# Kernel optimization log

Measured on AMD Instinct MI355X. Metric: run time of the kernel, lower is better.

## Reference

```python
import jax, jax.numpy as jnp
import numpy as np

NX, NY = 8, 1
IN_DELAY, FB_DELAY = 3, 3
MAX_DELAY = max(IN_DELAY, FB_DELAY)
HID = 64
NT, NG = 4096, 1024
IN_FEAT = (NX - NY) * (IN_DELAY + 1) + NY * (FB_DELAY + 1)  # 32


def setup_inputs() -> dict:
    key = jax.random.key(0)
    ks = jax.random.split(key, 10)
    s = lambda *sh: 0.05
    return {
        "x": jax.random.normal(ks[0], (NT, NG, NX), jnp.float32),
        "W_in": jax.random.normal(ks[1], (HID, IN_FEAT), jnp.float32) * 0.1,
        "b_in": jax.random.normal(ks[2], (HID,), jnp.float32) * 0.1,
        "W_ih": jax.random.normal(ks[3], (HID, HID), jnp.float32) * 0.1,
        "b_ih": jax.random.normal(ks[4], (HID,), jnp.float32) * 0.1,
        "W_hh": jax.random.normal(ks[5], (HID, HID), jnp.float32) * 0.1,
        "b_hh": jax.random.normal(ks[6], (HID,), jnp.float32) * 0.1,
        "W_out": jax.random.normal(ks[7], (NY, HID), jnp.float32) * 0.1,
        "b_out": jax.random.normal(ks[8], (NY,), jnp.float32) * 0.1,
    }


def _narx_forward(x, W_in, b_in, W_ih, b_ih, b_hh, W_out, b_out):
    nt = x.shape[0]
    # Source concat order: x0_t = x0[-1] then all x0[i], i=0..delay-1 (last slice duplicated).
    # x0 spans times [t-delay, t-1], so offsets relative to t are:
    off_x = jnp.array([-1] + list(range(-IN_DELAY, 0)))   # [4]
    off_y = jnp.array([-1] + list(range(-FB_DELAY, 0)))   # [4]
    ts = jnp.arange(MAX_DELAY, nt)                          # [T']
    # Gather delay windows: [T', n_off, ngrid, feat] -> [T', ngrid, n_off*feat]
    xw = x[ts[:, None] + off_x[None, :], :, :NX - NY]
    xw = jnp.transpose(xw, (0, 2, 1, 3)).reshape(xw.shape[0], xw.shape[2], -1)
    yw = x[ts[:, None] + off_y[None, :], :, NX - NY:]
    yw = jnp.transpose(yw, (0, 2, 1, 3)).reshape(yw.shape[0], yw.shape[2], -1)
    xt = jnp.concatenate([xw, yw], axis=-1)                 # [T', ngrid, IN_FEAT]
    h = jax.nn.relu(jnp.einsum('tgi,hi->tgh', xt, W_in) + b_in)
    # RNNCell called with hx=None each step in the source -> hidden is zeros every
    # call (W_hh contributes nothing); out = tanh(W_ih h + b_ih + b_hh).
    a = jnp.tanh(jnp.einsum('tgh,oh->tgo', h, W_ih) + b_ih + b_hh)
    y = jnp.einsum('tgh,oh->tgo', a, W_out) + b_out         # [T', ngrid, NY]
    # out[:max_delay] = x[:max_delay, :, -ny:]
    return jnp.concatenate([x[:MAX_DELAY, :, NX - NY:], y], axis=0)


def reference(x, W_in, b_in, W_ih, b_ih, W_hh, b_hh, W_out, b_out):
    # NestedNarx applies the shared Narx dl_model to every basin's series; with
    # the batched Narx this is exactly one call over all basins.
    return _narx_forward(x, W_in, b_in, W_ih, b_ih, b_hh, W_out, b_out)
```

## Files before the change

### kernel.cpp

```cpp
#include <hip/hip_runtime.h>
#include <hip/hip_bf16.h>


typedef __attribute__((ext_vector_type(8))) short bf16x8;
typedef __attribute__((ext_vector_type(4))) float f32x4;

__device__ __forceinline__ unsigned pk2(float lo, float hi) {
    unsigned r;
    asm("v_cvt_pk_bf16_f32 %0, %1, %2" : "=v"(r) : "v"(lo), "v"(hi));
    return r;
}

union BF8 { bf16x8 v; unsigned u[4]; uint4 q; };


__global__ __launch_bounds__(64) void narx_prep(
    const float* __restrict__ W_in, const float* __restrict__ b_in,
    const float* __restrict__ W_ih, const float* __restrict__ b_ih,
    const float* __restrict__ b_hh, const float* __restrict__ W_out,
    uint4* __restrict__ ws)
{
    const int lane = threadIdx.x;
    const int c = lane >> 4, pl = lane & 15;

    #pragma unroll
    for (int T = 0; T < 4; ++T) {
        const int r = ((pl >> 2) * 8) + (pl & 3) + (T & 1) * 4 + (T >> 1) * 32;
        const float* W = W_in + r * 32;
        float wr[8];
        if (c == 0) {
            #pragma unroll
            for (int j = 0; j < 7; ++j) wr[j] = W[j] + W[21 + j];
            wr[7] = W[28] + W[31];
        } else if (c == 1) {
            #pragma unroll
            for (int j = 0; j < 7; ++j) wr[j] = W[14 + j];
            wr[7] = W[30];
        } else if (c == 2) {
            #pragma unroll
            for (int j = 0; j < 7; ++j) wr[j] = W[7 + j];
            wr[7] = W[29];
        } else {
            wr[0] = b_in[r];
            #pragma unroll
            for (int j = 1; j < 8; ++j) wr[j] = 0.0f;
        }
        BF8 t;
        t.u[0] = pk2(wr[0], wr[1]); t.u[1] = pk2(wr[2], wr[3]);
        t.u[2] = pk2(wr[4], wr[5]); t.u[3] = pk2(wr[6], wr[7]);
        ws[lane*4 + T] = t.q;
    }

    #pragma unroll
    for (int k0 = 0; k0 < 2; ++k0)
    #pragma unroll
    for (int U = 0; U < 4; ++U) {
        const int r = ((pl >> 2) * 8) + (pl & 3) + (U & 1) * 4 + (U >> 1) * 32;
        const float* p = W_ih + r * 64 + 32*k0 + 8*c;
        float4 u0 = *(const float4*)p, u1 = *(const float4*)(p + 4);
        BF8 t;
        t.u[0] = pk2(u0.x, u0.y); t.u[1] = pk2(u0.z, u0.w);
        t.u[2] = pk2(u1.x, u1.y); t.u[3] = pk2(u1.z, u1.w);
        ws[256 + lane*8 + k0*4 + U] = t.q;
    }

    float4* wsf = (float4*)ws;
    #pragma unroll
    for (int U = 0; U < 4; ++U) {
        const int o = 8*c + 4*(U & 1) + 32*(U >> 1);
        wsf[768 + lane*4 + U] = make_float4(b_ih[o+0]+b_hh[o+0], b_ih[o+1]+b_hh[o+1],
                                            b_ih[o+2]+b_hh[o+2], b_ih[o+3]+b_hh[o+3]);
    }

    #pragma unroll
    for (int k0 = 0; k0 < 2; ++k0) {
        BF8 t;
        if (pl == 0) {
            const float* p = W_out + 32*k0 + 8*c;
            t.u[0] = pk2(p[0], p[1]); t.u[1] = pk2(p[2], p[3]);
            t.u[2] = pk2(p[4], p[5]); t.u[3] = pk2(p[6], p[7]);
        } else {
            t.u[0] = t.u[1] = t.u[2] = t.u[3] = 0u;
        }
        ws[1280 + lane*2 + k0] = t.q;
    }
}

__global__ __launch_bounds__(256, 2) void narx_main(
    const float* __restrict__ x, const uint4* __restrict__ ws,
    const float* __restrict__ b_out, float* __restrict__ out)
{
    __shared__ unsigned short F[4][128][32];

    const int nwg  = gridDim.x;
    const int orig = blockIdx.x;
    const int q8 = nwg >> 3, r8 = nwg & 7;
    const int xcd = orig & 7, inner = orig >> 3;
    const int b = (xcd < r8 ? xcd * (q8 + 1) : r8 * (q8 + 1) + (xcd - r8) * q8) + inner;

    const int lane = threadIdx.x & 63;
    const int w    = threadIdx.x >> 6;
    const int c    = lane >> 4;
    const int pl   = lane & 15;
    const int pt0  = 3072 + b * 512 + w * 128;

    bf16x8 wa[4];
    #pragma unroll
    for (int T = 0; T < 4; ++T) { BF8 t; t.q = ws[lane*4 + T]; wa[T] = t.v; }
    bf16x8 wi[2][4];
    #pragma unroll
    for (int k0 = 0; k0 < 2; ++k0)
    #pragma unroll
    for (int U = 0; U < 4; ++U) { BF8 t; t.q = ws[256 + lane*8 + k0*4 + U]; wi[k0][U] = t.v; }
    bf16x8 woa[2];
    #pragma unroll
    for (int k0 = 0; k0 < 2; ++k0) { BF8 t; t.q = ws[1280 + lane*2 + k0]; woa[k0] = t.v; }
    const float4* wsf = (const float4*)ws;
    f32x4 bias2[4];
    #pragma unroll
    for (int U = 0; U < 4; ++U) {
        float4 v = wsf[768 + lane*4 + U];
        bias2[U] = f32x4{v.x, v.y, v.z, v.w};
    }
    const float bout = b_out[0];
    const f32x4 cy = {c == 0 ? bout : 0.f, 0.f, 0.f, 0.f};
    const f32x4 zero = {0.f, 0.f, 0.f, 0.f};

    const float4* xr = (const float4*)x;
    {
        const int p0 = pt0 + lane, p1 = pt0 + 64 + lane;
        const int t0 = p0 >> 10, g0v = p0 & 1023;
        const int t1 = p1 >> 10, g1v = p1 & 1023;
        const size_t a1 = ((size_t)(t0-1)*1024 + g0v)*2, a2 = ((size_t)(t0-2)*1024 + g0v)*2,
                     a3 = ((size_t)(t0-3)*1024 + g0v)*2;
        const size_t d1a = ((size_t)(t1-1)*1024 + g1v)*2, d2a = ((size_t)(t1-2)*1024 + g1v)*2,
                     d3a = ((size_t)(t1-3)*1024 + g1v)*2;
        float4 A0 = xr[a1],  A1 = xr[a1+1],  B0 = xr[a2],  B1 = xr[a2+1],
               C0 = xr[a3],  C1 = xr[a3+1];
        float4 D0 = xr[d1a], D1 = xr[d1a+1], E0 = xr[d2a], E1 = xr[d2a+1],
               G0 = xr[d3a], G1 = xr[d3a+1];
        const int s = (lane >> 1) & 3;
        uint4* Fr0 = (uint4*)&F[w][lane][0];
        Fr0[0 ^ s] = make_uint4(pk2(A0.x,A0.y), pk2(A0.z,A0.w), pk2(A1.x,A1.y), pk2(A1.z,A1.w));
        Fr0[1 ^ s] = make_uint4(pk2(B0.x,B0.y), pk2(B0.z,B0.w), pk2(B1.x,B1.y), pk2(B1.z,B1.w));
        Fr0[2 ^ s] = make_uint4(pk2(C0.x,C0.y), pk2(C0.z,C0.w), pk2(C1.x,C1.y), pk2(C1.z,C1.w));
        Fr0[3 ^ s] = make_uint4(0x00003f80u, 0u, 0u, 0u);
        uint4* Fr1 = (uint4*)&F[w][64 + lane][0];
        Fr1[0 ^ s] = make_uint4(pk2(D0.x,D0.y), pk2(D0.z,D0.w), pk2(D1.x,D1.y), pk2(D1.z,D1.w));
        Fr1[1 ^ s] = make_uint4(pk2(E0.x,E0.y), pk2(E0.z,E0.w), pk2(E1.x,E1.y), pk2(E1.z,E1.w));
        Fr1[2 ^ s] = make_uint4(pk2(G0.x,G0.y), pk2(G0.z,G0.w), pk2(G1.x,G1.y), pk2(G1.z,G1.w));
        Fr1[3 ^ s] = make_uint4(0x00003f80u, 0u, 0u, 0u);
    }
    asm volatile("s_waitcnt lgkmcnt(0)" ::: "memory");
    __builtin_amdgcn_sched_barrier(0);

    asm volatile("" : "+v"(wa[0]), "+v"(wa[1]), "+v"(wa[2]), "+v"(wa[3]),
                      "+v"(wi[0][0]), "+v"(wi[0][1]), "+v"(wi[0][2]), "+v"(wi[0][3]),
                      "+v"(wi[1][0]), "+v"(wi[1][1]), "+v"(wi[1][2]), "+v"(wi[1][3]),
                      "+v"(bias2[0]), "+v"(bias2[1]), "+v"(bias2[2]), "+v"(bias2[3]),
                      "+v"(woa[0]), "+v"(woa[1]));

    const int s_rd = (pl >> 1) & 3;
    bf16x8 bf1 = *(bf16x8*)&F[w][pl][(c ^ s_rd) * 8];

    #pragma unroll 2
    for (int rb = 0; rb < 8; ++rb) {
        const int m0 = pt0 + rb * 16;

        f32x4 d1[4];
        #pragma unroll
        for (int T = 0; T < 4; ++T)
            d1[T] = __builtin_amdgcn_mfma_f32_16x16x32_bf16(wa[T], bf1, zero, 0, 0, 0);

        {
            const int rn = (rb < 7) ? rb + 1 : 7;
            bf1 = *(bf16x8*)&F[w][rn*16 + pl][(c ^ s_rd) * 8];
        }

        BF8 bh0, bh1;
        bh0.u[0] = pk2(fmaxf(d1[0][0],0.f), fmaxf(d1[0][1],0.f));
        bh0.u[1] = pk2(fmaxf(d1[0][2],0.f), fmaxf(d1[0][3],0.f));
        bh0.u[2] = pk2(fmaxf(d1[1][0],0.f), fmaxf(d1[1][1],0.f));
        bh0.u[3] = pk2(fmaxf(d1[1][2],0.f), fmaxf(d1[1][3],0.f));
        bh1.u[0] = pk2(fmaxf(d1[2][0],0.f), fmaxf(d1[2][1],0.f));
        bh1.u[1] = pk2(fmaxf(d1[2][2],0.f), fmaxf(d1[2][3],0.f));
        bh1.u[2] = pk2(fmaxf(d1[3][0],0.f), fmaxf(d1[3][1],0.f));
        bh1.u[3] = pk2(fmaxf(d1[3][2],0.f), fmaxf(d1[3][3],0.f));

        f32x4 d2[4];
        #pragma unroll
        for (int U = 0; U < 4; ++U) {
            d2[U] = __builtin_amdgcn_mfma_f32_16x16x32_bf16(wi[0][U], bh0.v, bias2[U], 0, 0, 0);
            d2[U] = __builtin_amdgcn_mfma_f32_16x16x32_bf16(wi[1][U], bh1.v, d2[U],   0, 0, 0);
        }

        f32x4 av[4];
        #pragma unroll
        for (int U = 0; U < 4; ++U) {
            f32x4 z;
            z[0] = __builtin_amdgcn_fmed3f(d2[U][0], -4.f, 4.f);
            z[1] = __builtin_amdgcn_fmed3f(d2[U][1], -4.f, 4.f);
            z[2] = __builtin_amdgcn_fmed3f(d2[U][2], -4.f, 4.f);
            z[3] = __builtin_amdgcn_fmed3f(d2[U][3], -4.f, 4.f);
            f32x4 p2  = z * z;
            f32x4 num = z * (p2 * (p2 + 105.f) + 945.f);
            f32x4 den = p2 * (p2 * 15.f + 420.f) + 945.f;
            f32x4 r;
            r[0] = __builtin_amdgcn_rcpf(den[0]);
            r[1] = __builtin_amdgcn_rcpf(den[1]);
            r[2] = __builtin_amdgcn_rcpf(den[2]);
            r[3] = __builtin_amdgcn_rcpf(den[3]);
            av[U] = num * r;
        }
        BF8 pb0, pb1;
        pb0.u[0] = pk2(av[0][0], av[0][1]); pb0.u[1] = pk2(av[0][2], av[0][3]);
        pb0.u[2] = pk2(av[1][0], av[1][1]); pb0.u[3] = pk2(av[1][2], av[1][3]);
        pb1.u[0] = pk2(av[2][0], av[2][1]); pb1.u[1] = pk2(av[2][2], av[2][3]);
        pb1.u[2] = pk2(av[3][0], av[3][1]); pb1.u[3] = pk2(av[3][2], av[3][3]);

        f32x4 dy;
        dy = __builtin_amdgcn_mfma_f32_16x16x32_bf16(woa[0], pb0.v, cy, 0, 0, 0);
        dy = __builtin_amdgcn_mfma_f32_16x16x32_bf16(woa[1], pb1.v, dy, 0, 0, 0);

        if (lane < 16)
            out[m0 + lane] = dy[0];
    }
}

__global__ __launch_bounds__(256) void narx_pass(const float* __restrict__ x, float* __restrict__ out) {
    const int i = blockIdx.x * 256 + threadIdx.x;
    out[i] = x[i * 8 + 7];
}

extern "C" void kernel_launch(void* const* d_in, const int* in_sizes, int n_in,
                              void* d_out, int out_size, void* d_ws, size_t ws_size,
                              hipStream_t stream) {
    const float* x     = (const float*)d_in[0];
    const float* W_in  = (const float*)d_in[1];
    const float* b_in  = (const float*)d_in[2];
    const float* W_ih  = (const float*)d_in[3];
    const float* b_ih  = (const float*)d_in[4];
    const float* b_hh  = (const float*)d_in[6];
    const float* W_out = (const float*)d_in[7];
    const float* b_out = (const float*)d_in[8];
    float* out = (float*)d_out;
    uint4* ws = (uint4*)d_ws;

    narx_prep<<<1, 64, 0, stream>>>(W_in, b_in, W_ih, b_ih, b_hh, W_out, ws);
    narx_main<<<8186, 256, 0, stream>>>(x, ws, b_out, out);
    narx_pass<<<12, 256, 0, stream>>>(x, out);
}
```

Measured before the change: 112.7 us.

## Load x windows directly into MFMA operand registers and use exp-based tanh

Drops the LDS staging of the delayed input windows. Each lane now loads its own delay slice of x from global memory straight into the MFMA B-operand registers, prefetching one row block ahead, and sets the bias slot in the fourth chunk. The Padé tanh approximation with clamping is replaced by a tanh computed from exp2 and a reciprocal, which cuts VALU work. The risk is more scattered global loads per lane and less latency hiding than the upfront batched load had.

```diff
diff --git a/kernel.cpp b/kernel.cpp
--- a/kernel.cpp
+++ b/kernel.cpp
@@ -90,8 +90,6 @@
     const float* __restrict__ x, const uint4* __restrict__ ws,
     const float* __restrict__ b_out, float* __restrict__ out)
 {
-    __shared__ unsigned short F[4][128][32];
-
     const int nwg  = gridDim.x;
     const int orig = blockIdx.x;
     const int q8 = nwg >> 3, r8 = nwg & 7;
@@ -99,10 +97,9 @@
     const int b = (xcd < r8 ? xcd * (q8 + 1) : r8 * (q8 + 1) + (xcd - r8) * q8) + inner;
 
     const int lane = threadIdx.x & 63;
-    const int w    = threadIdx.x >> 6;
     const int c    = lane >> 4;
     const int pl   = lane & 15;
-    const int pt0  = 3072 + b * 512 + w * 128;
+    const int pt0  = 3072 + b * 512 + (int)(threadIdx.x >> 6) * 128;
 
     bf16x8 wa[4];
     #pragma unroll
@@ -125,34 +122,6 @@
     const float bout = b_out[0];
     const f32x4 cy = {c == 0 ? bout : 0.f, 0.f, 0.f, 0.f};
     const f32x4 zero = {0.f, 0.f, 0.f, 0.f};
-
-    const float4* xr = (const float4*)x;
-    {
-        const int p0 = pt0 + lane, p1 = pt0 + 64 + lane;
-        const int t0 = p0 >> 10, g0v = p0 & 1023;
-        const int t1 = p1 >> 10, g1v = p1 & 1023;
-        const size_t a1 = ((size_t)(t0-1)*1024 + g0v)*2, a2 = ((size_t)(t0-2)*1024 + g0v)*2,
-                     a3 = ((size_t)(t0-3)*1024 + g0v)*2;
-        const size_t d1a = ((size_t)(t1-1)*1024 + g1v)*2, d2a = ((size_t)(t1-2)*1024 + g1v)*2,
-                     d3a = ((size_t)(t1-3)*1024 + g1v)*2;
-        float4 A0 = xr[a1],  A1 = xr[a1+1],  B0 = xr[a2],  B1 = xr[a2+1],
-               C0 = xr[a3],  C1 = xr[a3+1];
-        float4 D0 = xr[d1a], D1 = xr[d1a+1], E0 = xr[d2a], E1 = xr[d2a+1],
-               G0 = xr[d3a], G1 = xr[d3a+1];
-        const int s = (lane >> 1) & 3;
-        uint4* Fr0 = (uint4*)&F[w][lane][0];
-        Fr0[0 ^ s] = make_uint4(pk2(A0.x,A0.y), pk2(A0.z,A0.w), pk2(A1.x,A1.y), pk2(A1.z,A1.w));
-        Fr0[1 ^ s] = make_uint4(pk2(B0.x,B0.y), pk2(B0.z,B0.w), pk2(B1.x,B1.y), pk2(B1.z,B1.w));
-        Fr0[2 ^ s] = make_uint4(pk2(C0.x,C0.y), pk2(C0.z,C0.w), pk2(C1.x,C1.y), pk2(C1.z,C1.w));
-        Fr0[3 ^ s] = make_uint4(0x00003f80u, 0u, 0u, 0u);
-        uint4* Fr1 = (uint4*)&F[w][64 + lane][0];
-        Fr1[0 ^ s] = make_uint4(pk2(D0.x,D0.y), pk2(D0.z,D0.w), pk2(D1.x,D1.y), pk2(D1.z,D1.w));
-        Fr1[1 ^ s] = make_uint4(pk2(E0.x,E0.y), pk2(E0.z,E0.w), pk2(E1.x,E1.y), pk2(E1.z,E1.w));
-        Fr1[2 ^ s] = make_uint4(pk2(G0.x,G0.y), pk2(G0.z,G0.w), pk2(G1.x,G1.y), pk2(G1.z,G1.w));
-        Fr1[3 ^ s] = make_uint4(0x00003f80u, 0u, 0u, 0u);
-    }
-    asm volatile("s_waitcnt lgkmcnt(0)" ::: "memory");
-    __builtin_amdgcn_sched_barrier(0);
 
     asm volatile("" : "+v"(wa[0]), "+v"(wa[1]), "+v"(wa[2]), "+v"(wa[3]),
                       "+v"(wi[0][0]), "+v"(wi[0][1]), "+v"(wi[0][2]), "+v"(wi[0][3]),
@@ -160,22 +129,33 @@
                       "+v"(bias2[0]), "+v"(bias2[1]), "+v"(bias2[2]), "+v"(bias2[3]),
                       "+v"(woa[0]), "+v"(woa[1]));
 
-    const int s_rd = (pl >> 1) & 3;
-    bf16x8 bf1 = *(bf16x8*)&F[w][pl][(c ^ s_rd) * 8];
-
-    #pragma unroll 2
+    const int tw  = pt0 >> 10, g0w = pt0 & 1023;
+    const int dly = (c < 3) ? c : 0;
+    const float4* pbase = (const float4*)x + ((size_t)(tw - 1 - dly) * 1024 + g0w + pl) * 2;
+    const bool c3 = (c == 3);
+
+    float4 P0 = pbase[0], P1 = pbase[1];
+
+    #pragma unroll
     for (int rb = 0; rb < 8; ++rb) {
         const int m0 = pt0 + rb * 16;
+        float4 C0 = P0, C1 = P1;
+        if (rb < 7) { P0 = pbase[(rb + 1) * 32]; P1 = pbase[(rb + 1) * 32 + 1]; }
+
+        BF8 tv;
+        {
+            unsigned k0 = pk2(C0.x, C0.y), k1 = pk2(C0.z, C0.w);
+            unsigned k2 = pk2(C1.x, C1.y), k3 = pk2(C1.z, C1.w);
+            tv.u[0] = c3 ? 0x00003f80u : k0;
+            tv.u[1] = c3 ? 0u : k1;
+            tv.u[2] = c3 ? 0u : k2;
+            tv.u[3] = c3 ? 0u : k3;
+        }
 
         f32x4 d1[4];
         #pragma unroll
         for (int T = 0; T < 4; ++T)
-            d1[T] = __builtin_amdgcn_mfma_f32_16x16x32_bf16(wa[T], bf1, zero, 0, 0, 0);
-
-        {
-            const int rn = (rb < 7) ? rb + 1 : 7;
-            bf1 = *(bf16x8*)&F[w][rn*16 + pl][(c ^ s_rd) * 8];
-        }
+            d1[T] = __builtin_amdgcn_mfma_f32_16x16x32_bf16(wa[T], tv.v, zero, 0, 0, 0);
 
         BF8 bh0, bh1;
         bh0.u[0] = pk2(fmaxf(d1[0][0],0.f), fmaxf(d1[0][1],0.f));
@@ -197,20 +177,12 @@
         f32x4 av[4];
         #pragma unroll
         for (int U = 0; U < 4; ++U) {
-            f32x4 z;
-            z[0] = __builtin_amdgcn_fmed3f(d2[U][0], -4.f, 4.f);
-            z[1] = __builtin_amdgcn_fmed3f(d2[U][1], -4.f, 4.f);
-            z[2] = __builtin_amdgcn_fmed3f(d2[U][2], -4.f, 4.f);
-            z[3] = __builtin_amdgcn_fmed3f(d2[U][3], -4.f, 4.f);
-            f32x4 p2  = z * z;
-            f32x4 num = z * (p2 * (p2 + 105.f) + 945.f);
-            f32x4 den = p2 * (p2 * 15.f + 420.f) + 945.f;
-            f32x4 r;
-            r[0] = __builtin_amdgcn_rcpf(den[0]);
-            r[1] = __builtin_amdgcn_rcpf(den[1]);
-            r[2] = __builtin_amdgcn_rcpf(den[2]);
-            r[3] = __builtin_amdgcn_rcpf(den[3]);
-            av[U] = num * r;
+            #pragma unroll
+            for (int j = 0; j < 4; ++j) {
+                float e  = __builtin_amdgcn_exp2f(d2[U][j] * 2.885390081777927f);
+                float rc = __builtin_amdgcn_rcpf(e + 1.0f);
+                av[U][j] = fmaf(-2.0f, rc, 1.0f);
+            }
         }
         BF8 pb0, pb1;
         pb0.u[0] = pk2(av[0][0], av[0][1]); pb0.u[1] = pk2(av[0][2], av[0][3]);
```

New measurement: 119.9 us. 6.4% more time.
